# Kernel tuning notes

Hardware: AMD Instinct MI355X
Metric: run time of the kernel (lower is better)

## Reference

```python
import jax, jax.numpy as jnp
import numpy as np

EMBED_DIM = 512
NUM_HEADS = 8
HEAD_DIM = EMBED_DIM // NUM_HEADS
PAIR_BONUS = 2.0
MIN_SEPARATION = 3
PAIRING_MATRIX = jnp.array([
    [0, 1, 0, 0, 0],
    [1, 0, 1, 0, 0],
    [0, 1, 0, 1, 0],
    [0, 0, 1, 0, 0],
    [0, 0, 0, 0, 0],
], dtype=jnp.float32)


def setup_inputs() -> dict:
    key = jax.random.key(0)
    ks = jax.random.split(key, 12)
    B, S, E = 8, 1024, EMBED_DIM
    scale = 1.0 / np.sqrt(E)
    inp = {
        "query": jax.random.normal(ks[0], (B, S, E), dtype=jnp.float32),
        "key": jax.random.normal(ks[1], (B, S, E), dtype=jnp.float32),
        "value": jax.random.normal(ks[2], (B, S, E), dtype=jnp.float32),
        "nucleotide_sequence": jax.random.randint(ks[3], (B, S), 0, 5, dtype=jnp.int32),
        "key_padding_mask": jnp.zeros((B, S), dtype=bool),
        "Wq": jax.random.normal(ks[4], (E, E), dtype=jnp.float32) * scale,
        "bq": jnp.zeros((E,), dtype=jnp.float32),
        "Wk": jax.random.normal(ks[5], (E, E), dtype=jnp.float32) * scale,
        "bk": jnp.zeros((E,), dtype=jnp.float32),
        "Wv": jax.random.normal(ks[6], (E, E), dtype=jnp.float32) * scale,
        "bv": jnp.zeros((E,), dtype=jnp.float32),
        "Wo": jax.random.normal(ks[7], (E, E), dtype=jnp.float32) * scale,
        "bo": jnp.zeros((E,), dtype=jnp.float32),
    }
    return inp


def reference(query, key, value, nucleotide_sequence, key_padding_mask,
              Wq, bq, Wk, bk, Wv, bv, Wo, bo):
    B, T, E = query.shape
    S = key.shape[1]
    H, D = NUM_HEADS, HEAD_DIM
    scaling = D ** -0.5

    # projections -> (B, H, L, D)
    q = (query @ Wq + bq).reshape(B, T, H, D).transpose(0, 2, 1, 3)
    k = (key @ Wk + bk).reshape(B, S, H, D).transpose(0, 2, 1, 3)
    v = (value @ Wv + bv).reshape(B, S, H, D).transpose(0, 2, 1, 3)

    attn = jnp.einsum('bhtd,bhsd->bhts', q, k) * scaling  # (B,H,T,S)

    # base-pairing bias: gather into 5x5 table, masked by min separation
    pos = jnp.arange(S)
    sep_ok = (jnp.abs(pos[:, None] - pos[None, :]) >= MIN_SEPARATION).astype(jnp.float32)
    pairing = PAIRING_MATRIX[nucleotide_sequence[:, :, None], nucleotide_sequence[:, None, :]]  # (B,S,S)
    pair_bonus = pairing * sep_ok[None] * PAIR_BONUS
    attn = attn + pair_bonus[:, None, :, :]

    # key padding mask -> -inf
    attn = jnp.where(key_padding_mask[:, None, None, :], -jnp.inf, attn)

    attn_probs = jax.nn.softmax(attn, axis=-1)
    out = jnp.einsum('bhts,bhsd->bhtd', attn_probs, v)
    out = out.transpose(0, 2, 1, 3).reshape(B, T, E)
    out = out @ Wo + bo
    return out, attn_probs
```

## Files before the change

kernel.cpp:

```cpp
#include <hip/hip_runtime.h>
#include <hip/hip_bf16.h>
#include <stdint.h>


typedef float  f32x4  __attribute__((ext_vector_type(4)));
typedef short  s16x8  __attribute__((ext_vector_type(8)));

__device__ __forceinline__ ushort f2bf(float f) {
  union { float f; uint32_t u; } v; v.f = f;
  uint32_t u = v.u;
  return (ushort)((u + 0x7FFF + ((u >> 16) & 1)) >> 16);
}

__device__ __forceinline__ float bf2f(uint32_t u) {
  union { uint32_t u; float f; } v; v.u = u << 16;
  return v.f;
}

__device__ __forceinline__ f32x4 mfma16(s16x8 a, s16x8 b, f32x4 c) {
  return __builtin_amdgcn_mfma_f32_16x16x32_bf16(a, b, c, 0, 0, 0);
}

__device__ __forceinline__ void gl_lds16(const void* g, void* l) {
  typedef __attribute__((address_space(1))) const void gvoid;
  typedef __attribute__((address_space(3))) void lvoid;
  __builtin_amdgcn_global_load_lds((gvoid*)(uintptr_t)g,
                                   (lvoid*)(uint32_t)(uintptr_t)l, 16, 0, 0);
}

__global__ __launch_bounds__(256) void k_convert_w(
    const float* __restrict__ Wq, const float* __restrict__ Wk,
    const float* __restrict__ Wv, const float* __restrict__ Wo,
    ushort* __restrict__ WT, ushort* __restrict__ WoT) {
  int idx = blockIdx.x * 256 + threadIdx.x;
  int row = idx >> 9;
  int k = idx & 511;
  if (row < 1536) {
    const float* W = (row < 512) ? Wq : (row < 1024 ? Wk : Wv);
    int n = row & 511;
    WT[row * 512 + k] = f2bf(W[k * 512 + n]);
  } else {
    int n = row - 1536;
    WoT[n * 512 + k] = f2bf(Wo[k * 512 + n]);
  }
}

__global__ __launch_bounds__(256) void k_gemm_qkv(
    const float* __restrict__ Aq, const float* __restrict__ Ak,
    const float* __restrict__ Av, const ushort* __restrict__ WT,
    const float* __restrict__ bq, const float* __restrict__ bk,
    const float* __restrict__ bv, ushort* __restrict__ Y) {
  __shared__ ushort As[128 * 64];
  __shared__ ushort Bs[128 * 64];
  const int id = blockIdx.x;
  const int xcd = id & 7, slot = id >> 3;
  const int mb = xcd * 8 + slot / 12;
  const int nb = slot % 12;
  const int mat = nb >> 2;
  const float* A    = (mat == 0) ? Aq : (mat == 1 ? Ak : Av);
  const float* bias = (mat == 0) ? bq : (mat == 1 ? bk : bv);
  const int tid = threadIdx.x;
  const int w = tid >> 6, l = tid & 63;
  const int wr = (w >> 1) * 64, wc = (w & 1) * 64;
  const int lr = l & 15, lg = l >> 4;
  const int srow = l >> 3, sslot = (l & 7) ^ srow;

  f32x4 acc[4][4];
#pragma unroll
  for (int i = 0; i < 4; i++)
#pragma unroll
    for (int j = 0; j < 4; j++) acc[i][j] = (f32x4){0.f, 0.f, 0.f, 0.f};

  for (int kk = 0; kk < 8; kk++) {
    const int k0 = kk * 64;
#pragma unroll
    for (int it = 0; it < 8; it++) {
      int s2 = it * 256 + tid;
      int row = s2 >> 4;
      int k4 = (s2 & 15) * 4;
      float4 v = *reinterpret_cast<const float4*>(
          &A[(size_t)(mb * 128 + row) * 512 + k0 + k4]);
      uint64_t p = (uint64_t)f2bf(v.x) | ((uint64_t)f2bf(v.y) << 16) |
                   ((uint64_t)f2bf(v.z) << 32) | ((uint64_t)f2bf(v.w) << 48);
      int boff = row * 128 + ((k4 * 2) ^ ((row & 7) << 4));
      *reinterpret_cast<uint64_t*>((char*)As + boff) = p;
    }
#pragma unroll
    for (int it = 0; it < 4; it++) {
      int g8 = it * 4 + w;
      int row = g8 * 8 + srow;
      gl_lds16(&WT[(size_t)(nb * 128 + row) * 512 + k0 + sslot * 8], &Bs[g8 * 512]);
    }
    __syncthreads();
#pragma unroll
    for (int ks = 0; ks < 2; ks++) {
      s16x8 af[4], bfr[4];
#pragma unroll
      for (int mt = 0; mt < 4; mt++) {
        int row = wr + mt * 16 + lr;
        af[mt] = *reinterpret_cast<const s16x8*>(
            (char*)As + row * 128 + ((ks * 64 + lg * 16) ^ ((row & 7) << 4)));
      }
#pragma unroll
      for (int nt = 0; nt < 4; nt++) {
        int row = wc + nt * 16 + lr;
        bfr[nt] = *reinterpret_cast<const s16x8*>(
            (char*)Bs + row * 128 + ((ks * 64 + lg * 16) ^ ((row & 7) << 4)));
      }
#pragma unroll
      for (int mt = 0; mt < 4; mt++)
#pragma unroll
        for (int nt = 0; nt < 4; nt++)
          acc[mt][nt] = mfma16(af[mt], bfr[nt], acc[mt][nt]);
    }
    __syncthreads();
  }
  const int ncb = nb * 128;
#pragma unroll
  for (int nt = 0; nt < 4; nt++) {
    int gcol = ncb + wc + nt * 16 + lr;
    float bv_ = bias[gcol & 511];
#pragma unroll
    for (int mt = 0; mt < 4; mt++) {
#pragma unroll
      for (int r = 0; r < 4; r++) {
        int grow = mb * 128 + wr + mt * 16 + lg * 4 + r;
        Y[(size_t)grow * 1536 + gcol] = f2bf(acc[mt][nt][r] + bv_);
      }
    }
  }
}

__global__ __launch_bounds__(256) void k_transpose_v(
    const ushort* __restrict__ Y, ushort* __restrict__ vT) {
  __shared__ ushort T[64 * 64];
  const int sc = blockIdx.x;
  const int bh = blockIdx.y;
  const int b = bh >> 3, h = bh & 7;
  const int s0 = sc * 64;
  const int tid = threadIdx.x;
#pragma unroll
  for (int it = 0; it < 2; it++) {
    int slot = it * 256 + tid;
    int srw = slot >> 3;
    int i16 = (slot & 7) * 16;
    int4 v = *reinterpret_cast<const int4*>(
        &Y[(size_t)(b * 1024 + s0 + srw) * 1536 + 1024 + h * 64 + (slot & 7) * 8]);
    *reinterpret_cast<int4*>((char*)T + srw * 128 + (i16 ^ ((srw & 7) << 4))) = v;
  }
  __syncthreads();
  const int d = tid >> 2;
  const int sseg = (tid & 3) * 16;
  int pk[8];
#pragma unroll
  for (int j = 0; j < 8; j++) {
    int s0l = sseg + 2 * j;
    uint32_t a = *reinterpret_cast<const ushort*>(
        (char*)T + s0l * 128 + ((d * 2) ^ ((s0l & 7) << 4)));
    uint32_t bb = *reinterpret_cast<const ushort*>(
        (char*)T + (s0l + 1) * 128 + ((d * 2) ^ (((s0l + 1) & 7) << 4)));
    pk[j] = (int)(a | (bb << 16));
  }
  ushort* dst = &vT[(size_t)(bh * 64 + d) * 1024 + s0 + sseg];
  int4 o0 = {pk[0], pk[1], pk[2], pk[3]};
  int4 o1 = {pk[4], pk[5], pk[6], pk[7]};
  *reinterpret_cast<int4*>(dst) = o0;
  *reinterpret_cast<int4*>(dst + 8) = o1;
}

__global__ __launch_bounds__(256, 4) void k_attention(
    const ushort* __restrict__ Y, const ushort* __restrict__ vT,
    const int* __restrict__ seq, const unsigned char* __restrict__ mask,
    float* __restrict__ probs, ushort* __restrict__ AO) {
  __shared__ ushort Kb[2][4096];
  __shared__ ushort Vb[2][4096];
  __shared__ ushort Qb[1024];
  __shared__ ushort Pb[16 * 72];
  __shared__ ushort seqm[1024];
  __shared__ float rinv_s[16];
  float* Rbuf = reinterpret_cast<float*>(&Kb[0][0]);

  const int id = blockIdx.x;
  const int xcd = id & 7, slot = id >> 3;
  const int bh = xcd * 8 + (slot >> 6);
  const int tb = slot & 63;
  const int b = bh >> 3, h = bh & 7;
  const int tid = threadIdx.x;
  const int w = tid >> 6, l = tid & 63;
  const int lr = l & 15, lg = l >> 4;
  const int sc_ = w * 16;
  const int srw = sc_ + lr;
  const int srow = l >> 3, sslot = (l & 7) ^ srow;

#pragma unroll
  for (int it = 0; it < 4; it++) {
    int s = it * 256 + tid;
    seqm[s] = (ushort)(seq[b * 1024 + s] | (mask[b * 1024 + s] ? 0x100 : 0));
  }
#pragma unroll
  for (int it = 0; it < 2; it++) {
    int g8 = it * 4 + w;
    int row = g8 * 8 + srow;
    gl_lds16(&Y[(size_t)(b * 1024 + row) * 1536 + 512 + h * 64 + sslot * 8],
             &Kb[0][g8 * 512]);
    gl_lds16(&vT[(size_t)(bh * 64 + row) * 1024 + sslot * 8], &Vb[0][g8 * 512]);
  }
  if (w < 2) {
    gl_lds16(&Y[(size_t)(b * 1024 + tb * 16 + w * 8 + srow) * 1536 + h * 64 +
                sslot * 8],
             &Qb[w * 512]);
  }
  __syncthreads();

  s16x8 qf0 = *reinterpret_cast<const s16x8*>(
      (char*)Qb + lr * 128 + ((lg * 16) ^ ((lr & 7) << 4)));
  s16x8 qf1 = *reinterpret_cast<const s16x8*>(
      (char*)Qb + lr * 128 + ((64 + lg * 16) ^ ((lr & 7) << 4)));
  int seqt[4];
#pragma unroll
  for (int r = 0; r < 4; r++) seqt[r] = seqm[tb * 16 + lg * 4 + r] & 255;

  uint2 pe[16];
  float psum[4] = {0.f, 0.f, 0.f, 0.f};
  f32x4 oacc = (f32x4){0.f, 0.f, 0.f, 0.f};

#pragma unroll
  for (int c = 0; c < 16; c++) {
    if (c < 15) {
#pragma unroll
      for (int it = 0; it < 2; it++) {
        int g8 = it * 4 + w;
        int row = g8 * 8 + srow;
        gl_lds16(&Y[(size_t)(b * 1024 + (c + 1) * 64 + row) * 1536 + 512 +
                    h * 64 + sslot * 8],
                 &Kb[(c + 1) & 1][g8 * 512]);
        gl_lds16(&vT[(size_t)(bh * 64 + row) * 1024 + (c + 1) * 64 + sslot * 8],
                 &Vb[(c + 1) & 1][g8 * 512]);
      }
    }
    s16x8 kf0 = *reinterpret_cast<const s16x8*>(
        (char*)&Kb[c & 1][0] + srw * 128 + ((lg * 16) ^ ((srw & 7) << 4)));
    s16x8 kf1 = *reinterpret_cast<const s16x8*>(
        (char*)&Kb[c & 1][0] + srw * 128 + ((64 + lg * 16) ^ ((srw & 7) << 4)));
    f32x4 facc = (f32x4){0.f, 0.f, 0.f, 0.f};
    facc = mfma16(qf0, kf0, facc);
    facc = mfma16(qf1, kf1, facc);

    const int sg = c * 64 + srw;
    const int sm = seqm[sg];
    const int ss = sm & 255;
    const bool msk = (sm & 0x100) != 0;
    ushort eb[4];
#pragma unroll
    for (int r = 0; r < 4; r++) {
      int tg = tb * 16 + lg * 4 + r;
      int dsep = tg - sg; dsep = dsep < 0 ? -dsep : dsep;
      int dnt = seqt[r] - ss; dnt = dnt < 0 ? -dnt : dnt;
      bool bon = (dnt == 1 && seqt[r] <= 3 && ss <= 3 && dsep >= 3);
      float v = facc[r] * 0.125f + (bon ? 2.0f : 0.0f);
      float ee = msk ? 0.0f : __expf(v - 12.0f);
      psum[r] += ee;
      eb[r] = f2bf(ee);
      Pb[(lg * 4 + r) * 72 + srw] = eb[r];
    }
    pe[c].x = (uint32_t)eb[0] | ((uint32_t)eb[1] << 16);
    pe[c].y = (uint32_t)eb[2] | ((uint32_t)eb[3] << 16);
    __syncthreads();

#pragma unroll
    for (int ks = 0; ks < 2; ks++) {
      s16x8 paf = *reinterpret_cast<const s16x8*>(&Pb[lr * 72 + ks * 32 + lg * 8]);
      s16x8 vb = *reinterpret_cast<const s16x8*>(
          (char*)&Vb[c & 1][0] + srw * 128 +
          ((ks * 64 + lg * 16) ^ ((srw & 7) << 4)));
      oacc = mfma16(paf, vb, oacc);
    }
    __syncthreads();
  }

#pragma unroll
  for (int r = 0; r < 4; r++) Rbuf[((w * 4 + lg) * 4 + r) * 16 + lr] = psum[r];
  __syncthreads();
  {
    int row = tid >> 4, j = tid & 15;
    int lgr = row >> 2, rr = row & 3;
    float s = 0.f;
#pragma unroll
    for (int i = 0; i < 4; i++) {
      int wj = j >> 2;
      int lrj = (j & 3) * 4 + i;
      s += Rbuf[((wj * 4 + lgr) * 4 + rr) * 16 + lrj];
    }
#pragma unroll
    for (int off = 1; off < 16; off <<= 1) s += __shfl_xor(s, off);
    if (j == 0) rinv_s[row] = 1.0f / s;
  }
  __syncthreads();
  float rv[4];
#pragma unroll
  for (int r = 0; r < 4; r++) rv[r] = rinv_s[lg * 4 + r];

#pragma unroll
  for (int r = 0; r < 4; r++) {
    int t = tb * 16 + lg * 4 + r;
    AO[((size_t)b * 1024 + t) * 512 + h * 64 + sc_ + lr] = f2bf(oacc[r] * rv[r]);
  }

#pragma unroll
  for (int r = 0; r < 4; r++) {
    float* prow = &probs[((size_t)bh * 1024 + tb * 16 + lg * 4 + r) * 1024 + srw];
#pragma unroll
    for (int c = 0; c < 16; c++) {
      uint32_t u = (r < 2) ? pe[c].x : pe[c].y;
      u = (u >> ((r & 1) * 16)) & 0xffffu;
      prow[c * 64] = bf2f(u) * rv[r];
    }
  }
}

__global__ __launch_bounds__(256) void k_gemm_o(
    const ushort* __restrict__ AO, const ushort* __restrict__ WoT,
    const float* __restrict__ bo, float* __restrict__ out) {
  __shared__ ushort As[128 * 64];
  __shared__ ushort Bs[128 * 64];
  const int id = blockIdx.x;
  const int xcd = id & 7, slot = id >> 3;
  const int mb = xcd * 8 + (slot >> 2);
  const int nb = slot & 3;
  const int tid = threadIdx.x;
  const int w = tid >> 6, l = tid & 63;
  const int wr = (w >> 1) * 64, wc = (w & 1) * 64;
  const int lr = l & 15, lg = l >> 4;
  const int srow = l >> 3, sslot = (l & 7) ^ srow;

  f32x4 acc[4][4];
#pragma unroll
  for (int i = 0; i < 4; i++)
#pragma unroll
    for (int j = 0; j < 4; j++) acc[i][j] = (f32x4){0.f, 0.f, 0.f, 0.f};

  for (int kk = 0; kk < 8; kk++) {
    const int k0 = kk * 64;
#pragma unroll
    for (int it = 0; it < 4; it++) {
      int g8 = it * 4 + w;
      int row = g8 * 8 + srow;
      gl_lds16(&AO[(size_t)(mb * 128 + row) * 512 + k0 + sslot * 8], &As[g8 * 512]);
      gl_lds16(&WoT[(size_t)(nb * 128 + row) * 512 + k0 + sslot * 8], &Bs[g8 * 512]);
    }
    __syncthreads();
#pragma unroll
    for (int ks = 0; ks < 2; ks++) {
      s16x8 af[4], bfr[4];
#pragma unroll
      for (int mt = 0; mt < 4; mt++) {
        int row = wr + mt * 16 + lr;
        af[mt] = *reinterpret_cast<const s16x8*>(
            (char*)As + row * 128 + ((ks * 64 + lg * 16) ^ ((row & 7) << 4)));
      }
#pragma unroll
      for (int nt = 0; nt < 4; nt++) {
        int row = wc + nt * 16 + lr;
        bfr[nt] = *reinterpret_cast<const s16x8*>(
            (char*)Bs + row * 128 + ((ks * 64 + lg * 16) ^ ((row & 7) << 4)));
      }
#pragma unroll
      for (int mt = 0; mt < 4; mt++)
#pragma unroll
        for (int nt = 0; nt < 4; nt++)
          acc[mt][nt] = mfma16(af[mt], bfr[nt], acc[mt][nt]);
    }
    __syncthreads();
  }
  const int ncb = nb * 128;
#pragma unroll
  for (int nt = 0; nt < 4; nt++) {
    int gcol = ncb + wc + nt * 16 + lr;
    float bv_ = bo[gcol];
#pragma unroll
    for (int mt = 0; mt < 4; mt++) {
#pragma unroll
      for (int r = 0; r < 4; r++) {
        int grow = mb * 128 + wr + mt * 16 + lg * 4 + r;
        out[(size_t)grow * 512 + gcol] = acc[mt][nt][r] + bv_;
      }
    }
  }
}

extern "C" void kernel_launch(void* const* d_in, const int* in_sizes, int n_in,
                              void* d_out, int out_size, void* d_ws, size_t ws_size,
                              hipStream_t stream) {
  (void)in_sizes; (void)n_in; (void)out_size; (void)ws_size;
  const float* query = (const float*)d_in[0];
  const float* key   = (const float*)d_in[1];
  const float* value = (const float*)d_in[2];
  const int* seq     = (const int*)d_in[3];
  const unsigned char* mask = (const unsigned char*)d_in[4];
  const float* Wq = (const float*)d_in[5];
  const float* bq = (const float*)d_in[6];
  const float* Wk = (const float*)d_in[7];
  const float* bk = (const float*)d_in[8];
  const float* Wv = (const float*)d_in[9];
  const float* bv = (const float*)d_in[10];
  const float* Wo = (const float*)d_in[11];
  const float* bo = (const float*)d_in[12];

  float* out = (float*)d_out;
  float* probs = out + (size_t)8 * 1024 * 512;

  char* ws = (char*)d_ws;
  ushort* Y   = (ushort*)(ws);
  ushort* WT  = (ushort*)(ws + 25165824);
  ushort* WoT = (ushort*)(ws + 26738688);
  ushort* vT  = (ushort*)(ws + 27262976);
  ushort* AO  = (ushort*)(ws + 35651584);

  k_convert_w<<<4096, 256, 0, stream>>>(Wq, Wk, Wv, Wo, WT, WoT);
  k_gemm_qkv<<<768, 256, 0, stream>>>(query, key, value, WT, bq, bk, bv, Y);
  k_transpose_v<<<dim3(16, 64), 256, 0, stream>>>(Y, vT);
  k_attention<<<4096, 256, 0, stream>>>(Y, vT, seq, mask, probs, AO);
  k_gemm_o<<<256, 256, 0, stream>>>(AO, WoT, bo, out);
}
```

Measured before the change: 219.6 us.

## Use explicit vmcnt waits and LDS-staged float4 stores for attention probs

Replaces __syncthreads with hand-placed s_waitcnt vmcnt/lgkmcnt plus s_barrier, so the loop only waits for the current K/V tile's async global-to-LDS loads and the next tile's prefetch stays in flight. Each wave now loads a contiguous pair of 8-row groups, which changes the per-wave load ordering. The probability write-out is staged through LDS (reusing the K buffer) and stored as coalesced float4 rows instead of scattered 4-byte stores. This adds two barriers per chunk in the epilogue and depends on the vmcnt(4) count matching the number of outstanding loads issued.

```diff
diff --git a/kernel.cpp b/kernel.cpp
--- a/kernel.cpp
+++ b/kernel.cpp
@@ -26,6 +26,20 @@
   typedef __attribute__((address_space(3))) void lvoid;
   __builtin_amdgcn_global_load_lds((gvoid*)(uintptr_t)g,
                                    (lvoid*)(uint32_t)(uintptr_t)l, 16, 0, 0);
+}
+
+__device__ __forceinline__ void vwait4() {
+  asm volatile("s_waitcnt vmcnt(4)" ::: "memory");
+  __builtin_amdgcn_sched_barrier(0);
+}
+__device__ __forceinline__ void vwait0() {
+  asm volatile("s_waitcnt vmcnt(0)" ::: "memory");
+  __builtin_amdgcn_sched_barrier(0);
+}
+__device__ __forceinline__ void bar_lds() {
+  asm volatile("s_waitcnt lgkmcnt(0)" ::: "memory");
+  __builtin_amdgcn_s_barrier();
+  __builtin_amdgcn_sched_barrier(0);
 }
 
 __global__ __launch_bounds__(256) void k_convert_w(
@@ -199,7 +213,7 @@
   }
 #pragma unroll
   for (int it = 0; it < 2; it++) {
-    int g8 = it * 4 + w;
+    int g8 = w * 2 + it;
     int row = g8 * 8 + srow;
     gl_lds16(&Y[(size_t)(b * 1024 + row) * 1536 + 512 + h * 64 + sslot * 8],
              &Kb[0][g8 * 512]);
@@ -229,7 +243,7 @@
     if (c < 15) {
 #pragma unroll
       for (int it = 0; it < 2; it++) {
-        int g8 = it * 4 + w;
+        int g8 = w * 2 + it;
         int row = g8 * 8 + srow;
         gl_lds16(&Y[(size_t)(b * 1024 + (c + 1) * 64 + row) * 1536 + 512 +
                     h * 64 + sslot * 8],
@@ -237,6 +251,9 @@
         gl_lds16(&vT[(size_t)(bh * 64 + row) * 1024 + (c + 1) * 64 + sslot * 8],
                  &Vb[(c + 1) & 1][g8 * 512]);
       }
+      vwait4();
+    } else {
+      vwait0();
     }
     s16x8 kf0 = *reinterpret_cast<const s16x8*>(
         (char*)&Kb[c & 1][0] + srw * 128 + ((lg * 16) ^ ((srw & 7) << 4)));
@@ -265,7 +282,7 @@
     }
     pe[c].x = (uint32_t)eb[0] | ((uint32_t)eb[1] << 16);
     pe[c].y = (uint32_t)eb[2] | ((uint32_t)eb[3] << 16);
-    __syncthreads();
+    bar_lds();
 
 #pragma unroll
     for (int ks = 0; ks < 2; ks++) {
@@ -275,7 +292,7 @@
           ((ks * 64 + lg * 16) ^ ((srw & 7) << 4)));
       oacc = mfma16(paf, vb, oacc);
     }
-    __syncthreads();
+    bar_lds();
   }
 
 #pragma unroll
@@ -306,15 +323,21 @@
     AO[((size_t)b * 1024 + t) * 512 + h * 64 + sc_ + lr] = f2bf(oacc[r] * rv[r]);
   }
 
-#pragma unroll
-  for (int r = 0; r < 4; r++) {
-    float* prow = &probs[((size_t)bh * 1024 + tb * 16 + lg * 4 + r) * 1024 + srw];
-#pragma unroll
-    for (int c = 0; c < 16; c++) {
+  float* Pf = reinterpret_cast<float*>(&Kb[0][0]);
+  const int prow_ = tid >> 4, pj = tid & 15;
+  float* pdst_base = &probs[((size_t)bh * 1024 + tb * 16 + prow_) * 1024 + pj * 4];
+#pragma unroll
+  for (int c = 0; c < 16; c++) {
+#pragma unroll
+    for (int r = 0; r < 4; r++) {
       uint32_t u = (r < 2) ? pe[c].x : pe[c].y;
       u = (u >> ((r & 1) * 16)) & 0xffffu;
-      prow[c * 64] = bf2f(u) * rv[r];
-    }
+      Pf[(lg * 4 + r) * 68 + srw] = bf2f(u) * rv[r];
+    }
+    bar_lds();
+    float4 p4 = *reinterpret_cast<const float4*>(&Pf[prow_ * 68 + pj * 4]);
+    *reinterpret_cast<float4*>(pdst_base + c * 64) = p4;
+    bar_lds();
   }
 }
 
```

Measured after the change: 217.1 us. About the same (-1.1%).
